# Kernel optimization log

Hardware: AMD Instinct MI355X
Metric: run time of the kernel (lower is better)

The kernel has to match this reference:

```python
import jax, jax.numpy as jnp
import numpy as np

EPS = 1e-06


def setup_inputs() -> dict:
    key = jax.random.key(0)
    kq, kk, kv = jax.random.split(key, 3)
    B, H, T, P = 2, 8, 1024, 64
    Q = jax.random.normal(kq, (B, H, T, P), dtype=jnp.float32)
    K = jax.random.normal(kk, (B, H, T, P), dtype=jnp.float32)
    V = jax.random.normal(kv, (B, H, T, P), dtype=jnp.float32)
    return {"Q": Q, "K": K, "V": V}


def _scan_attention(Q, K, V):
    Q_feat = jnp.exp(Q)                                  # (B,H,T,P)
    K_feat = jnp.exp(K)                                  # (B,H,T,P)
    m0 = jnp.log(K_feat)                                 # (B,H,T,P)
    N0 = jnp.einsum('bhtp,bhtn->bhtpn', V, K_feat)       # (B,H,T,P,P) matrix state
    D0 = K_feat                                          # (B,H,T,P)

    def combine(x, y):
        m_x, N_x, D_x = x
        m_y, N_y, D_y = y
        m_new = jnp.maximum(m_x, m_y)
        scale_x = jnp.exp(m_x - m_new)
        scale_y = jnp.exp(m_y - m_new)
        N_new = N_x * scale_x[..., None] + N_y * scale_y[..., None]
        D_new = D_x * scale_x + D_y * scale_y
        return (m_new, N_new, D_new)

    m_cum, num_cum, denom_cum = jax.lax.associative_scan(combine, (m0, N0, D0), axis=2)

    Y_num = jnp.einsum('bhtp,bhtpq->bhtq', Q_feat, num_cum)   # (B,H,T,P)
    Y_den = jnp.einsum('bhtp,bhtp->bht', Q_feat, denom_cum)   # (B,H,T)
    Y = Y_num / (Y_den[..., None] + EPS)
    B, H, T, P = Q.shape
    return Y.transpose(0, 2, 1, 3).reshape(B, T, H * P)


def reference(Q, K, V):
    return _scan_attention(Q, K, V)
```

## Files before the change

kernel.cpp:

```cpp
#include <hip/hip_runtime.h>
#include <hip/hip_bf16.h>

#define TDIM 1024
#define PDIM 64
#define BHN  16
#define SCH  8
#define NSC  128

typedef __bf16 bf16_t;
typedef bf16_t bf16x8 __attribute__((ext_vector_type(8)));
typedef float  floatx4 __attribute__((ext_vector_type(4)));

__device__ __forceinline__ floatx4 mfma16(bf16x8 a, bf16x8 b, floatx4 c) {
    return __builtin_amdgcn_mfma_f32_16x16x32_bf16(a, b, c, 0, 0, 0);
}

__global__ __launch_bounds__(64) void prep_kernel(
        const float* __restrict__ K, const float* __restrict__ V,
        bf16_t* __restrict__ U, bf16_t* __restrict__ Kft,
        float2* __restrict__ stats) {
    int bh = blockIdx.x >> 6;
    int c  = blockIdx.x & 63;
    int p  = threadIdx.x;
    size_t base = (size_t)bh * TDIM * PDIM;
    int t0 = c * 16;

    float kq[16], vv[16];
#pragma unroll
    for (int i = 0; i < 16; ++i) {
        kq[i] = K[base + (size_t)(t0 + i) * PDIM + p];
        vv[i] = V[base + (size_t)(t0 + i) * PDIM + p];
    }

    __shared__ bf16_t ek_t[16][PDIM + 4];
    float m0 = -INFINITY, s0 = 0.f, m1 = -INFINITY, s1 = 0.f;
#pragma unroll
    for (int i = 0; i < 16; ++i) {
        float e = __expf(kq[i]);
        if (i < 8) { m0 = fmaxf(m0, kq[i]); s0 += e * e; }
        else       { m1 = fmaxf(m1, kq[i]); s1 += e * e; }
        U[base + (size_t)(t0 + i) * PDIM + p] = (bf16_t)(vv[i] * e);
        ek_t[i][p] = (bf16_t)e;
    }
    stats[((size_t)(bh << 7) + 2 * c + 0) * PDIM + p] = make_float2(m0, s0);
    stats[((size_t)(bh << 7) + 2 * c + 1) * PDIM + p] = make_float2(m1, s1);
    __syncthreads();

    int hi = p >> 4, tl = p & 15;
#pragma unroll
    for (int it = 0; it < 16; ++it) {
        int q = it * 4 + hi;
        Kft[((size_t)bh * PDIM + q) * TDIM + t0 + tl] = ek_t[tl][q];
    }
}

__global__ __launch_bounds__(512) void featattn_kernel(
        const float* __restrict__ Q, const float* __restrict__ K,
        const bf16_t* __restrict__ U, const bf16_t* __restrict__ Kft,
        const float2* __restrict__ stats, float* __restrict__ out) {
    int bh  = blockIdx.x & 15;
    int i   = blockIdx.x >> 4;
    int tid = threadIdx.x;
    int wave = tid >> 6, lane = tid & 63;
    int lq = lane & 15, qd = lane >> 4;
    int sub = wave & 3;
    int par = wave >> 2;
    int b = bh >> 3, h = bh & 7;

    __shared__ bf16_t Wt[64][72];
    __shared__ bf16_t Ut[2][64][72];
    __shared__ bf16_t Kt[2][64][72];
    __shared__ __align__(16) char ctyraw[8 * 16 * 72 * 2];
    __shared__ float denb[64];
    bf16_t (*Ct)[16][72]  = (bf16_t (*)[16][72])ctyraw;
    float  (*Yred)[16][68] = (float (*)[16][68])ctyraw;
    float2 (*Pt)[64]       = (float2 (*)[64])ctyraw;

    size_t base = (size_t)bh * TDIM * PDIM;
    size_t kftb = (size_t)bh * PDIM * TDIM;
    int row = tid >> 3, c8 = (tid & 7) << 3;

    int4 pu0 = *(const int4*)(U + base + (size_t)(0 * 64 + row) * PDIM + c8);
    int4 pk0 = *(const int4*)(Kft + kftb + (size_t)row * TDIM + 0 * 64 + c8);
    int4 pu1 = *(const int4*)(U + base + (size_t)(1 * 64 + row) * PDIM + c8);
    int4 pk1 = *(const int4*)(Kft + kftb + (size_t)row * TDIM + 1 * 64 + c8);

    {
        int t0 = i * 64 + wave * 8;
        float kr[8], qr[8];
#pragma unroll
        for (int j = 0; j < 8; ++j) {
            kr[j] = K[base + (size_t)(t0 + j) * PDIM + lane];
            qr[j] = Q[base + (size_t)(t0 + j) * PDIM + lane];
        }

        const float2* st2 = stats + (size_t)(bh << 7) * PDIM + lane;
        int lim = 8 * i;
        float pm0 = -INFINITY, pm1 = -INFINITY, pm2 = -INFINITY, pm3 = -INFINITY;
        float ps0 = 0.f, ps1 = 0.f, ps2 = 0.f, ps3 = 0.f;
        int cc = wave;
        for (; cc + 24 < lim; cc += 32) {
            float2 v0 = st2[(size_t)(cc +  0) * PDIM];
            float2 v1 = st2[(size_t)(cc +  8) * PDIM];
            float2 v2 = st2[(size_t)(cc + 16) * PDIM];
            float2 v3 = st2[(size_t)(cc + 24) * PDIM];
            pm0 = fmaxf(pm0, v0.x); ps0 += v0.y;
            pm1 = fmaxf(pm1, v1.x); ps1 += v1.y;
            pm2 = fmaxf(pm2, v2.x); ps2 += v2.y;
            pm3 = fmaxf(pm3, v3.x); ps3 += v3.y;
        }
        for (; cc < lim; cc += 8) {
            float2 v = st2[(size_t)cc * PDIM];
            pm0 = fmaxf(pm0, v.x); ps0 += v.y;
        }
        Pt[wave][lane] = make_float2(fmaxf(fmaxf(pm0, pm1), fmaxf(pm2, pm3)),
                                     (ps0 + ps1) + (ps2 + ps3));
        __syncthreads();

        float m = -INFINITY, s = 0.f;
#pragma unroll
        for (int g = 0; g < 8; ++g) {
            float2 v = Pt[g][lane];
            m = fmaxf(m, v.x); s += v.y;
        }
        for (int bc = lim; bc < lim + wave; ++bc) {
            float2 v = st2[(size_t)bc * PDIM];
            m = fmaxf(m, v.x); s += v.y;
        }

        float d[8];
#pragma unroll
        for (int j = 0; j < 8; ++j) {
            m = fmaxf(m, kr[j]);
            float e = __expf(kr[j]);
            s += e * e;
            float wv = __expf(qr[j] - m);
            Wt[wave * 8 + j][lane] = (bf16_t)wv;
            d[j] = wv * s;
        }
#pragma unroll
        for (int off = 32; off > 0; off >>= 1)
#pragma unroll
            for (int j = 0; j < 8; ++j) d[j] += __shfl_xor(d[j], off);
        if (lane == 0) {
#pragma unroll
            for (int j = 0; j < 8; ++j) denb[wave * 8 + j] = d[j];
        }
    }
    __syncthreads();

    bf16x8 a0 = *(const bf16x8*)&Wt[sub * 16 + lq][qd * 8];
    bf16x8 a1 = *(const bf16x8*)&Wt[sub * 16 + lq][32 + qd * 8];

    floatx4 acc[4];
#pragma unroll
    for (int j = 0; j < 4; ++j) acc[j] = (floatx4){0.f, 0.f, 0.f, 0.f};

    int niter = (i >> 1) + 1;
    for (int kt2 = 0; kt2 < niter; ++kt2) {
        __syncthreads();
        *(int4*)&Ut[0][row][c8] = pu0;
        *(int4*)&Kt[0][row][c8] = pk0;
        *(int4*)&Ut[1][row][c8] = pu1;
        *(int4*)&Kt[1][row][c8] = pk1;
        if (kt2 + 1 < niter) {
            int ktn = 2 * kt2 + 2;
            int ktn1 = ktn + 1 > 15 ? 15 : ktn + 1;
            pu0 = *(const int4*)(U + base + (size_t)(ktn * 64 + row) * PDIM + c8);
            pk0 = *(const int4*)(Kft + kftb + (size_t)row * TDIM + ktn * 64 + c8);
            pu1 = *(const int4*)(U + base + (size_t)(ktn1 * 64 + row) * PDIM + c8);
            pk1 = *(const int4*)(Kft + kftb + (size_t)row * TDIM + ktn1 * 64 + c8);
        }
        __syncthreads();

        int kt = 2 * kt2 + par;
        if (kt <= i) {
            floatx4 cc4[4];
#pragma unroll
            for (int j = 0; j < 4; ++j) {
                bf16x8 b0 = *(const bf16x8*)&Ut[par][j * 16 + lq][qd * 8];
                bf16x8 b1 = *(const bf16x8*)&Ut[par][j * 16 + lq][32 + qd * 8];
                floatx4 t = (floatx4){0.f, 0.f, 0.f, 0.f};
                t = mfma16(a0, b0, t);
                t = mfma16(a1, b1, t);
                cc4[j] = t;
            }
            int trow0 = i * 64 + sub * 16;
#pragma unroll
            for (int j = 0; j < 4; ++j) {
#pragma unroll
                for (int r = 0; r < 4; ++r) {
                    float v = cc4[j][r];
                    if (kt == i && (kt * 64 + j * 16 + lq) > (trow0 + qd * 4 + r))
                        v = 0.f;
                    Ct[wave][qd * 4 + r][j * 16 + lq] = (bf16_t)v;
                }
            }
            bf16x8 ca0 = *(const bf16x8*)&Ct[wave][lq][qd * 8];
            bf16x8 ca1 = *(const bf16x8*)&Ct[wave][lq][32 + qd * 8];
#pragma unroll
            for (int j = 0; j < 4; ++j) {
                bf16x8 kb0 = *(const bf16x8*)&Kt[par][j * 16 + lq][qd * 8];
                bf16x8 kb1 = *(const bf16x8*)&Kt[par][j * 16 + lq][32 + qd * 8];
                acc[j] = mfma16(ca0, kb0, acc[j]);
                acc[j] = mfma16(ca1, kb1, acc[j]);
            }
        }
    }

    __syncthreads();
    if (par == 1) {
#pragma unroll
        for (int j = 0; j < 4; ++j)
#pragma unroll
            for (int r = 0; r < 4; ++r)
                Yred[sub][qd * 4 + r][j * 16 + lq] = acc[j][r];
    }
    __syncthreads();
    if (par == 0) {
#pragma unroll
        for (int j = 0; j < 4; ++j) {
#pragma unroll
            for (int r = 0; r < 4; ++r) {
                int trow_l = sub * 16 + qd * 4 + r;
                int tg = i * 64 + trow_l;
                float y = acc[j][r] + Yred[sub][qd * 4 + r][j * 16 + lq];
                y = y / (denb[trow_l] + 1e-6f);
                out[((size_t)b * TDIM + tg) * (8 * PDIM) + h * PDIM + j * 16 + lq] = y;
            }
        }
    }
}

extern "C" void kernel_launch(void* const* d_in, const int* in_sizes, int n_in,
                              void* d_out, int out_size, void* d_ws, size_t ws_size,
                              hipStream_t stream) {
    const float* Q = (const float*)d_in[0];
    const float* K = (const float*)d_in[1];
    const float* V = (const float*)d_in[2];
    float* out = (float*)d_out;

    bf16_t* Uf   = (bf16_t*)d_ws;
    bf16_t* Kft  = Uf + (size_t)BHN * TDIM * PDIM;
    float2* stats = (float2*)(Kft + (size_t)BHN * TDIM * PDIM);

    prep_kernel<<<BHN * 64, 64, 0, stream>>>(K, V, Uf, Kft, stats);
    featattn_kernel<<<256, 512, 0, stream>>>(Q, K, Uf, Kft, stats, out);
}
```

Measured before the change: 84.50 us.

## Fuse prep and attention kernels into one cooperative launch with grid sync

```diff
diff --git a/kernel.cpp b/kernel.cpp
--- a/kernel.cpp
+++ b/kernel.cpp
@@ -1,11 +1,12 @@
 #include <hip/hip_runtime.h>
 #include <hip/hip_bf16.h>
+#include <hip/hip_cooperative_groups.h>
+
+namespace cg = cooperative_groups;
 
 #define TDIM 1024
 #define PDIM 64
 #define BHN  16
-#define SCH  8
-#define NSC  128
 
 typedef __bf16 bf16_t;
 typedef bf16_t bf16x8 __attribute__((ext_vector_type(8)));
@@ -15,49 +16,11 @@
     return __builtin_amdgcn_mfma_f32_16x16x32_bf16(a, b, c, 0, 0, 0);
 }
 
-__global__ __launch_bounds__(64) void prep_kernel(
-        const float* __restrict__ K, const float* __restrict__ V,
-        bf16_t* __restrict__ U, bf16_t* __restrict__ Kft,
-        float2* __restrict__ stats) {
-    int bh = blockIdx.x >> 6;
-    int c  = blockIdx.x & 63;
-    int p  = threadIdx.x;
-    size_t base = (size_t)bh * TDIM * PDIM;
-    int t0 = c * 16;
-
-    float kq[16], vv[16];
-#pragma unroll
-    for (int i = 0; i < 16; ++i) {
-        kq[i] = K[base + (size_t)(t0 + i) * PDIM + p];
-        vv[i] = V[base + (size_t)(t0 + i) * PDIM + p];
-    }
-
-    __shared__ bf16_t ek_t[16][PDIM + 4];
-    float m0 = -INFINITY, s0 = 0.f, m1 = -INFINITY, s1 = 0.f;
-#pragma unroll
-    for (int i = 0; i < 16; ++i) {
-        float e = __expf(kq[i]);
-        if (i < 8) { m0 = fmaxf(m0, kq[i]); s0 += e * e; }
-        else       { m1 = fmaxf(m1, kq[i]); s1 += e * e; }
-        U[base + (size_t)(t0 + i) * PDIM + p] = (bf16_t)(vv[i] * e);
-        ek_t[i][p] = (bf16_t)e;
-    }
-    stats[((size_t)(bh << 7) + 2 * c + 0) * PDIM + p] = make_float2(m0, s0);
-    stats[((size_t)(bh << 7) + 2 * c + 1) * PDIM + p] = make_float2(m1, s1);
-    __syncthreads();
-
-    int hi = p >> 4, tl = p & 15;
-#pragma unroll
-    for (int it = 0; it < 16; ++it) {
-        int q = it * 4 + hi;
-        Kft[((size_t)bh * PDIM + q) * TDIM + t0 + tl] = ek_t[tl][q];
-    }
-}
-
-__global__ __launch_bounds__(512) void featattn_kernel(
+__global__ __launch_bounds__(512) void fused_kernel(
         const float* __restrict__ Q, const float* __restrict__ K,
-        const bf16_t* __restrict__ U, const bf16_t* __restrict__ Kft,
-        const float2* __restrict__ stats, float* __restrict__ out) {
+        const float* __restrict__ V,
+        bf16_t* U, bf16_t* Kft, float2* stats,
+        float* __restrict__ out) {
     int bh  = blockIdx.x & 15;
     int i   = blockIdx.x >> 4;
     int tid = threadIdx.x;
@@ -79,6 +42,35 @@
     size_t base = (size_t)bh * TDIM * PDIM;
     size_t kftb = (size_t)bh * PDIM * TDIM;
     int row = tid >> 3, c8 = (tid & 7) << 3;
+
+    {
+        int slab = i * 8 + wave;
+        int t0p  = slab * 8;
+        float kq[8], vv[8];
+#pragma unroll
+        for (int j = 0; j < 8; ++j) {
+            kq[j] = K[base + (size_t)(t0p + j) * PDIM + lane];
+            vv[j] = V[base + (size_t)(t0p + j) * PDIM + lane];
+        }
+        float m = -INFINITY, s = 0.f;
+#pragma unroll
+        for (int j = 0; j < 8; ++j) {
+            float e = __expf(kq[j]);
+            m = fmaxf(m, kq[j]);
+            s += e * e;
+            U[base + (size_t)(t0p + j) * PDIM + lane] = (bf16_t)(vv[j] * e);
+            Ut[0][wave * 8 + j][lane] = (bf16_t)e;
+        }
+        stats[((size_t)(bh << 7) + slab) * PDIM + lane] = make_float2(m, s);
+        int hi = lane >> 3, tl = lane & 7;
+#pragma unroll
+        for (int it = 0; it < 8; ++it) {
+            int q = it * 8 + hi;
+            Kft[kftb + (size_t)q * TDIM + t0p + tl] = Ut[0][wave * 8 + tl][q];
+        }
+    }
+    __threadfence();
+    cg::this_grid().sync();
 
     int4 pu0 = *(const int4*)(U + base + (size_t)(0 * 64 + row) * PDIM + c8);
     int4 pk0 = *(const int4*)(Kft + kftb + (size_t)row * TDIM + 0 * 64 + c8);
@@ -244,6 +236,8 @@
     bf16_t* Kft  = Uf + (size_t)BHN * TDIM * PDIM;
     float2* stats = (float2*)(Kft + (size_t)BHN * TDIM * PDIM);
 
-    prep_kernel<<<BHN * 64, 64, 0, stream>>>(K, V, Uf, Kft, stats);
-    featattn_kernel<<<256, 512, 0, stream>>>(Q, K, Uf, Kft, stats, out);
+    void* args[] = {(void*)&Q, (void*)&K, (void*)&V,
+                    (void*)&Uf, (void*)&Kft, (void*)&stats, (void*)&out};
+    hipLaunchCooperativeKernel((const void*)fused_kernel,
+                               dim3(256), dim3(512), args, 0, stream);
 }
```

After: 191.5 us. +126.7%, slower.
